# Kernel optimization log

Hardware: AMD Instinct MI355X
Metric: run time of the kernel (lower is better)

The kernel has to match this reference:

```python
import jax, jax.numpy as jnp
import numpy as np

NUM_EMBEDDINGS = 512
EMBEDDING_DIM = 64
COMMITMENT_COST = 0.25


def setup_inputs() -> dict:
    key = jax.random.key(0)
    k1, k2 = jax.random.split(key)
    inputs = jax.random.normal(k1, (64, EMBEDDING_DIM, 32, 32), dtype=jnp.float32)
    # codebook initialized uniform(-1/K, 1/K) like the torch module
    bound = 1.0 / NUM_EMBEDDINGS
    embedding = jax.random.uniform(k2, (NUM_EMBEDDINGS, EMBEDDING_DIM),
                                   dtype=jnp.float32, minval=-bound, maxval=bound)
    return {"inputs": inputs, "embedding": embedding}


def reference(inputs, embedding):
    # NCHW -> NHWC
    x = jnp.transpose(inputs, (0, 2, 3, 1))
    B, H, W, D = x.shape
    K = embedding.shape[0]
    flat = x.reshape(-1, D)  # [N, D]
    # squared L2 distances to every codebook entry: [N, K]
    dist = (jnp.sum(flat * flat, axis=1, keepdims=True)
            + jnp.sum(embedding * embedding, axis=1)
            - 2.0 * flat @ embedding.T)
    idx = jnp.argmin(dist, axis=1)  # [N]
    # gather replaces one-hot @ codebook (same math)
    quantized = embedding[idx].reshape(B, H, W, D)
    e_latent_loss = jnp.mean((jax.lax.stop_gradient(quantized) - x) ** 2)
    q_latent_loss = jnp.mean((quantized - jax.lax.stop_gradient(x)) ** 2)
    loss = q_latent_loss + COMMITMENT_COST * e_latent_loss
    # straight-through estimator
    quantized_st = x + jax.lax.stop_gradient(quantized - x)
    # perplexity from code usage histogram (== mean of one-hot encodings)
    avg_probs = jnp.zeros((K,), dtype=x.dtype).at[idx].add(1.0) / idx.shape[0]
    perplexity = jnp.exp(-jnp.sum(avg_probs * jnp.log(avg_probs + 1e-10)))
    return (loss,
            jnp.transpose(quantized_st, (0, 3, 1, 2)),
            perplexity,
            quantized_st.reshape(B, -1))
```

## Files before the change

### kernel.cpp

```cpp
#include <hip/hip_runtime.h>


constexpr int DIM    = 64;
constexpr int KC     = 512;
constexpr int HW     = 1024;
constexpr int NPTS   = 65536;
constexpr int QELEMS = NPTS * DIM;

typedef float f32x16 __attribute__((ext_vector_type(16)));
typedef short bf16x8 __attribute__((ext_vector_type(8)));

__device__ inline unsigned short f2bf(float f) {
    unsigned u = __float_as_uint(f);
    u += 0x7FFF + ((u >> 16) & 1);
    return (unsigned short)(u >> 16);
}
__device__ inline float bf2f(unsigned short s) { return __uint_as_float(((unsigned)s) << 16); }

__device__ inline uint4 pack8(const unsigned short* s) {
    return make_uint4((unsigned)s[0] | ((unsigned)s[1] << 16),
                      (unsigned)s[2] | ((unsigned)s[3] << 16),
                      (unsigned)s[4] | ((unsigned)s[5] << 16),
                      (unsigned)s[6] | ((unsigned)s[7] << 16));
}

__global__ __launch_bounds__(256)
void vq_prep_kernel(const float* __restrict__ emb, unsigned short* __restrict__ EH)
{
    const int t = blockIdx.x * 256 + threadIdx.x;
    if (t < 4096) {
        const int c = t & 511, hb = t >> 9;
        const int d0 = 16 * (hb >> 1) + 4 * (hb & 1);
        const float* e = emb + (size_t)c * DIM;
        float4 v0 = *reinterpret_cast<const float4*>(e + d0);
        float4 v1 = *reinterpret_cast<const float4*>(e + d0 + 8);
        unsigned short s[8];
        s[0]=f2bf(-v0.x); s[1]=f2bf(-v0.y); s[2]=f2bf(-v0.z); s[3]=f2bf(-v0.w);
        s[4]=f2bf(-v1.x); s[5]=f2bf(-v1.y); s[6]=f2bf(-v1.z); s[7]=f2bf(-v1.w);
        *reinterpret_cast<uint4*>(EH + (size_t)(hb * KC + c) * 8) = pack8(s);
    } else if (t < 4608) {
        const int c = t - 4096;
        const float4* er = reinterpret_cast<const float4*>(emb + (size_t)c * DIM);
        float nrm = 0.f;
        #pragma unroll
        for (int i = 0; i < DIM / 4; ++i) {
            float4 v = er[i];
            nrm = fmaf(v.x,v.x,fmaf(v.y,v.y,fmaf(v.z,v.z,fmaf(v.w,v.w,nrm))));
        }
        float val = 0.5f + 0.5f * nrm;
        unsigned short nh = f2bf(val);
        unsigned short nl = f2bf(val - bf2f(nh));
        unsigned short ext[8] = {nh, nl, 0,0,0,0,0,0};
        unsigned short zer[8] = {0,0,0,0,0,0,0,0};
        *reinterpret_cast<uint4*>(EH + (size_t)(8 * KC + c) * 8) = pack8(ext);
        *reinterpret_cast<uint4*>(EH + (size_t)(9 * KC + c) * 8) = pack8(zer);
    }
}

__global__ __launch_bounds__(256, 4)
void vq_main_kernel(const float* __restrict__ x, const float* __restrict__ emb,
                    const unsigned short* __restrict__ EH,
                    int* __restrict__ hist, float* __restrict__ loss_accum,
                    float* __restrict__ out_nchw, float* __restrict__ out_flat)
{
    __shared__ unsigned wkeys[4][32];

    const int tid  = threadIdx.x;
    const int w    = tid >> 6, lane = tid & 63;
    const int lo   = lane & 31, hi = lane >> 5;
    const int pair = w >> 1,  pw  = w & 1;

    const int n0  = blockIdx.x * 64 + pair * 32;
    const int b   = n0 >> 10;
    const int hw0 = n0 & (HW - 1);

    bf16x8 BH[4], BL[4];
    float xnorm = 0.f;
    const float* xp = x + (size_t)b * (DIM * HW) + hw0 + lo;
    #pragma unroll
    for (int ks = 0; ks < 4; ++ks) {
        bf16x8 bh, bl;
        #pragma unroll
        for (int j = 0; j < 8; ++j) {
            const int d = 16 * ks + 4 * hi + (j & 3) + 8 * (j >> 2);
            float v = xp[(size_t)d * HW];
            xnorm = fmaf(v, v, xnorm);
            unsigned short h = f2bf(v);
            bh[j] = (short)h;
            bl[j] = (short)f2bf(v - bf2f(h));
        }
        BH[ks] = bh; BL[ks] = bl;
    }
    bf16x8 B1 = {(short)0x3F80, (short)0x3F80, 0,0,0,0,0,0};

    unsigned rkey = 0xFFFFFFFFu;
    const int cbase = pw * 256;
    #pragma unroll
    for (int cc = 0; cc < 4; ++cc) {
        const int c0 = cbase + 64 * cc;
        f32x16 a0 = {}, a1 = {};
        #pragma unroll
        for (int ks = 0; ks < 4; ++ks) {
            const int hb = 2 * ks + hi;
            bf16x8 A0 = *reinterpret_cast<const bf16x8*>(EH + (size_t)(hb * KC + c0 + lo) * 8);
            bf16x8 A1 = *reinterpret_cast<const bf16x8*>(EH + (size_t)(hb * KC + c0 + 32 + lo) * 8);
            a0 = __builtin_amdgcn_mfma_f32_32x32x16_bf16(A0, BH[ks], a0, 0, 0, 0);
            a1 = __builtin_amdgcn_mfma_f32_32x32x16_bf16(A1, BH[ks], a1, 0, 0, 0);
            a0 = __builtin_amdgcn_mfma_f32_32x32x16_bf16(A0, BL[ks], a0, 0, 0, 0);
            a1 = __builtin_amdgcn_mfma_f32_32x32x16_bf16(A1, BL[ks], a1, 0, 0, 0);
        }
        {
            const int hb = 8 + hi;
            bf16x8 N0 = *reinterpret_cast<const bf16x8*>(EH + (size_t)(hb * KC + c0 + lo) * 8);
            bf16x8 N1 = *reinterpret_cast<const bf16x8*>(EH + (size_t)(hb * KC + c0 + 32 + lo) * 8);
            a0 = __builtin_amdgcn_mfma_f32_32x32x16_bf16(N0, B1, a0, 0, 0, 0);
            a1 = __builtin_amdgcn_mfma_f32_32x32x16_bf16(N1, B1, a1, 0, 0, 0);
        }
        const unsigned kb0 = (unsigned)(c0 + 4 * hi), kb1 = kb0 + 32;
        unsigned m0 = 0xFFFFFFFFu, m1 = 0xFFFFFFFFu, m2 = 0xFFFFFFFFu, m3 = 0xFFFFFFFFu;
        #pragma unroll
        for (int r = 0; r < 16; ++r) {
            const unsigned kc = (unsigned)((r & 3) + 8 * (r >> 2));
            unsigned k0 = (__float_as_uint(a0[r]) & 0xFFFFFE00u) | (kb0 + kc);
            unsigned k1 = (__float_as_uint(a1[r]) & 0xFFFFFE00u) | (kb1 + kc);
            unsigned m  = min(k0, k1);
            if ((r & 3) == 0) m0 = min(m0, m);
            else if ((r & 3) == 1) m1 = min(m1, m);
            else if ((r & 3) == 2) m2 = min(m2, m);
            else m3 = min(m3, m);
        }
        rkey = min(rkey, min(min(m0, m1), min(m2, m3)));
    }

    rkey  = min(rkey, (unsigned)__shfl_xor((int)rkey, 32, 64));
    xnorm += __shfl_xor(xnorm, 32, 64);
    if (hi == 0) wkeys[w][lo] = rkey;
    __syncthreads();
    const unsigned fkey = min(wkeys[2 * pair][lo], wkeys[2 * pair + 1][lo]);

    if (pw == 0) {
        const int   code = (int)(fkey & 511u);
        const float v    = __uint_as_float(fkey & 0xFFFFFE00u);
        float ls = (hi == 0) ? (2.f * v - 1.f + xnorm) : 0.f;
        if (hi == 0) atomicAdd(&hist[code], 1);
        #pragma unroll
        for (int off = 32; off > 0; off >>= 1) ls += __shfl_down(ls, off, 64);
        if (lane == 0) atomicAdd(loss_accum, ls);
    }

    if (pw == 0) {
        const int p = lane >> 1, q = lane & 1;
        const int code = __shfl((int)fkey, p, 64) & 511;
        const float4* er = reinterpret_cast<const float4*>(emb + (size_t)code * DIM) + q * 8;
        float* ob = out_nchw + (size_t)b * (DIM * HW) + hw0 + p;
        #pragma unroll
        for (int j = 0; j < 8; ++j) {
            float4 vv = er[j];
            const int d = q * 32 + 4 * j;
            ob[(size_t)(d + 0) * HW] = vv.x;
            ob[(size_t)(d + 1) * HW] = vv.y;
            ob[(size_t)(d + 2) * HW] = vv.z;
            ob[(size_t)(d + 3) * HW] = vv.w;
        }
    } else {
        #pragma unroll
        for (int i = 0; i < 16; ++i) {
            const int p = 2 * i + hi;
            const int code = __shfl((int)fkey, p, 64) & 511;
            float2 vv = *reinterpret_cast<const float2*>(emb + (size_t)code * DIM + 2 * lo);
            *reinterpret_cast<float2*>(out_flat + (size_t)(n0 + p) * DIM + 2 * lo) = vv;
        }
    }
}

__global__ __launch_bounds__(512, 1)
void vq_finalize_kernel(const int* __restrict__ hist, const float* __restrict__ loss_accum,
                        float* __restrict__ out_loss, float* __restrict__ out_perp)
{
    __shared__ float wsum[8];
    const int tid = threadIdx.x;
    const float p = (float)hist[tid] * (1.0f / (float)NPTS);
    float t = p * logf(p + 1e-10f);
    #pragma unroll
    for (int off = 32; off > 0; off >>= 1)
        t += __shfl_down(t, off, 64);
    if ((tid & 63) == 0) wsum[tid >> 6] = t;
    __syncthreads();
    if (tid == 0) {
        float s = 0.f;
        #pragma unroll
        for (int w = 0; w < 8; ++w) s += wsum[w];
        *out_perp = expf(-s);
        *out_loss = (*loss_accum) * 1.25f / (float)QELEMS;
    }
}

extern "C" void kernel_launch(void* const* d_in, const int* in_sizes, int n_in,
                              void* d_out, int out_size, void* d_ws, size_t ws_size,
                              hipStream_t stream)
{
    const float* x   = (const float*)d_in[0];
    const float* emb = (const float*)d_in[1];
    float* out = (float*)d_out;

    float*          loss_accum = (float*)d_ws;
    int*            hist       = (int*)((char*)d_ws + 64);
    unsigned short* EH         = (unsigned short*)((char*)d_ws + 4096);

    hipMemsetAsync(d_ws, 0, 4096, stream);

    vq_prep_kernel<<<18, 256, 0, stream>>>(emb, EH);

    vq_main_kernel<<<NPTS / 64, 256, 0, stream>>>(x, emb, EH, hist, loss_accum,
                                                  out + 1, out + 2 + QELEMS);

    vq_finalize_kernel<<<1, 512, 0, stream>>>(hist, loss_accum, out, out + 1 + QELEMS);
}
```

Baseline: 126.3 us.

## Split VQ main kernel into argmin and output-writing kernels with LDS transpose

The fused kernel is split into an argmin kernel, which stores per-point codes to a workspace index buffer, and a separate outputs kernel that gathers codebook rows, writes the flat output, and transposes through padded shared memory for the NCHW output. The argmin kernel also hoists all x loads and codebook fragment loads ahead of the MFMA chain to expose more memory-level parallelism. This is meant to make the output stores more uniform and lighten register pressure in the compute kernel. In exchange it adds a kernel launch and an extra round trip of the index array through global memory.

```diff
diff --git a/kernel.cpp b/kernel.cpp
--- a/kernel.cpp
+++ b/kernel.cpp
@@ -58,10 +58,9 @@
 }
 
 __global__ __launch_bounds__(256, 4)
-void vq_main_kernel(const float* __restrict__ x, const float* __restrict__ emb,
-                    const unsigned short* __restrict__ EH,
-                    int* __restrict__ hist, float* __restrict__ loss_accum,
-                    float* __restrict__ out_nchw, float* __restrict__ out_flat)
+void vq_argmin_kernel(const float* __restrict__ x, const unsigned short* __restrict__ EH,
+                      int* __restrict__ idx, int* __restrict__ hist,
+                      float* __restrict__ loss_accum)
 {
     __shared__ unsigned wkeys[4][32];
 
@@ -74,16 +73,22 @@
     const int b   = n0 >> 10;
     const int hw0 = n0 & (HW - 1);
 
+    const float* xp = x + (size_t)b * (DIM * HW) + hw0 + lo;
+    float xv[32];
+    #pragma unroll
+    for (int ks = 0; ks < 4; ++ks)
+        #pragma unroll
+        for (int j = 0; j < 8; ++j)
+            xv[ks * 8 + j] = xp[(size_t)(16 * ks + 4 * hi + (j & 3) + 8 * (j >> 2)) * HW];
+
     bf16x8 BH[4], BL[4];
     float xnorm = 0.f;
-    const float* xp = x + (size_t)b * (DIM * HW) + hw0 + lo;
     #pragma unroll
     for (int ks = 0; ks < 4; ++ks) {
         bf16x8 bh, bl;
         #pragma unroll
         for (int j = 0; j < 8; ++j) {
-            const int d = 16 * ks + 4 * hi + (j & 3) + 8 * (j >> 2);
-            float v = xp[(size_t)d * HW];
+            float v = xv[ks * 8 + j];
             xnorm = fmaf(v, v, xnorm);
             unsigned short h = f2bf(v);
             bh[j] = (short)h;
@@ -98,24 +103,29 @@
     #pragma unroll
     for (int cc = 0; cc < 4; ++cc) {
         const int c0 = cbase + 64 * cc;
+        bf16x8 A0[5], A1[5];
+        #pragma unroll
+        for (int ks = 0; ks < 4; ++ks) {
+            const size_t base = (size_t)((2 * ks + hi) * KC + c0 + lo) * 8;
+            A0[ks] = *reinterpret_cast<const bf16x8*>(EH + base);
+            A1[ks] = *reinterpret_cast<const bf16x8*>(EH + base + 256);
+        }
+        {
+            const size_t base = (size_t)((8 + hi) * KC + c0 + lo) * 8;
+            A0[4] = *reinterpret_cast<const bf16x8*>(EH + base);
+            A1[4] = *reinterpret_cast<const bf16x8*>(EH + base + 256);
+        }
         f32x16 a0 = {}, a1 = {};
         #pragma unroll
         for (int ks = 0; ks < 4; ++ks) {
-            const int hb = 2 * ks + hi;
-            bf16x8 A0 = *reinterpret_cast<const bf16x8*>(EH + (size_t)(hb * KC + c0 + lo) * 8);
-            bf16x8 A1 = *reinterpret_cast<const bf16x8*>(EH + (size_t)(hb * KC + c0 + 32 + lo) * 8);
-            a0 = __builtin_amdgcn_mfma_f32_32x32x16_bf16(A0, BH[ks], a0, 0, 0, 0);
-            a1 = __builtin_amdgcn_mfma_f32_32x32x16_bf16(A1, BH[ks], a1, 0, 0, 0);
-            a0 = __builtin_amdgcn_mfma_f32_32x32x16_bf16(A0, BL[ks], a0, 0, 0, 0);
-            a1 = __builtin_amdgcn_mfma_f32_32x32x16_bf16(A1, BL[ks], a1, 0, 0, 0);
-        }
-        {
-            const int hb = 8 + hi;
-            bf16x8 N0 = *reinterpret_cast<const bf16x8*>(EH + (size_t)(hb * KC + c0 + lo) * 8);
-            bf16x8 N1 = *reinterpret_cast<const bf16x8*>(EH + (size_t)(hb * KC + c0 + 32 + lo) * 8);
-            a0 = __builtin_amdgcn_mfma_f32_32x32x16_bf16(N0, B1, a0, 0, 0, 0);
-            a1 = __builtin_amdgcn_mfma_f32_32x32x16_bf16(N1, B1, a1, 0, 0, 0);
-        }
+            a0 = __builtin_amdgcn_mfma_f32_32x32x16_bf16(A0[ks], BH[ks], a0, 0, 0, 0);
+            a1 = __builtin_amdgcn_mfma_f32_32x32x16_bf16(A1[ks], BH[ks], a1, 0, 0, 0);
+            a0 = __builtin_amdgcn_mfma_f32_32x32x16_bf16(A0[ks], BL[ks], a0, 0, 0, 0);
+            a1 = __builtin_amdgcn_mfma_f32_32x32x16_bf16(A1[ks], BL[ks], a1, 0, 0, 0);
+        }
+        a0 = __builtin_amdgcn_mfma_f32_32x32x16_bf16(A0[4], B1, a0, 0, 0, 0);
+        a1 = __builtin_amdgcn_mfma_f32_32x32x16_bf16(A1[4], B1, a1, 0, 0, 0);
+
         const unsigned kb0 = (unsigned)(c0 + 4 * hi), kb1 = kb0 + 32;
         unsigned m0 = 0xFFFFFFFFu, m1 = 0xFFFFFFFFu, m2 = 0xFFFFFFFFu, m3 = 0xFFFFFFFFu;
         #pragma unroll
@@ -132,44 +142,62 @@
         rkey = min(rkey, min(min(m0, m1), min(m2, m3)));
     }
 
-    rkey  = min(rkey, (unsigned)__shfl_xor((int)rkey, 32, 64));
+    rkey   = min(rkey, (unsigned)__shfl_xor((int)rkey, 32, 64));
     xnorm += __shfl_xor(xnorm, 32, 64);
     if (hi == 0) wkeys[w][lo] = rkey;
     __syncthreads();
-    const unsigned fkey = min(wkeys[2 * pair][lo], wkeys[2 * pair + 1][lo]);
 
     if (pw == 0) {
+        const unsigned fkey = min(wkeys[2 * pair][lo], wkeys[2 * pair + 1][lo]);
         const int   code = (int)(fkey & 511u);
         const float v    = __uint_as_float(fkey & 0xFFFFFE00u);
+        if (hi == 0) {
+            idx[n0 + lo] = code;
+            atomicAdd(&hist[code], 1);
+        }
         float ls = (hi == 0) ? (2.f * v - 1.f + xnorm) : 0.f;
-        if (hi == 0) atomicAdd(&hist[code], 1);
         #pragma unroll
         for (int off = 32; off > 0; off >>= 1) ls += __shfl_down(ls, off, 64);
         if (lane == 0) atomicAdd(loss_accum, ls);
     }
-
-    if (pw == 0) {
-        const int p = lane >> 1, q = lane & 1;
-        const int code = __shfl((int)fkey, p, 64) & 511;
-        const float4* er = reinterpret_cast<const float4*>(emb + (size_t)code * DIM) + q * 8;
+}
+
+__global__ __launch_bounds__(256)
+void vq_outputs_kernel(const float* __restrict__ emb, const int* __restrict__ idx,
+                       float* __restrict__ out_nchw, float* __restrict__ out_flat)
+{
+    __shared__ float rows[64 * 65];
+    __shared__ int   scode[64];
+
+    const int tid = threadIdx.x;
+    const int p0  = blockIdx.x * 64;
+    const int b   = p0 >> 10;
+    const int hw0 = p0 & (HW - 1);
+
+    if (tid < 64) scode[tid] = idx[p0 + tid];
+    __syncthreads();
+
+    {
+        const int p = tid >> 2, q = tid & 3;
+        const float4* er = reinterpret_cast<const float4*>(emb + (size_t)scode[p] * DIM) + q * 4;
+        float2* of = reinterpret_cast<float2*>(out_flat + (size_t)(p0 + p) * DIM + q * 16);
+        float*  dst = &rows[p * 65 + q * 16];
+        #pragma unroll
+        for (int i = 0; i < 4; ++i) {
+            float4 v = er[i];
+            of[2 * i]     = make_float2(v.x, v.y);
+            of[2 * i + 1] = make_float2(v.z, v.w);
+            dst[4 * i + 0] = v.x; dst[4 * i + 1] = v.y;
+            dst[4 * i + 2] = v.z; dst[4 * i + 3] = v.w;
+        }
+    }
+    __syncthreads();
+    {
+        const int p = tid & 63, d0 = (tid >> 6) * 16;
         float* ob = out_nchw + (size_t)b * (DIM * HW) + hw0 + p;
         #pragma unroll
-        for (int j = 0; j < 8; ++j) {
-            float4 vv = er[j];
-            const int d = q * 32 + 4 * j;
-            ob[(size_t)(d + 0) * HW] = vv.x;
-            ob[(size_t)(d + 1) * HW] = vv.y;
-            ob[(size_t)(d + 2) * HW] = vv.z;
-            ob[(size_t)(d + 3) * HW] = vv.w;
-        }
-    } else {
-        #pragma unroll
-        for (int i = 0; i < 16; ++i) {
-            const int p = 2 * i + hi;
-            const int code = __shfl((int)fkey, p, 64) & 511;
-            float2 vv = *reinterpret_cast<const float2*>(emb + (size_t)code * DIM + 2 * lo);
-            *reinterpret_cast<float2*>(out_flat + (size_t)(n0 + p) * DIM + 2 * lo) = vv;
-        }
+        for (int i = 0; i < 16; ++i)
+            ob[(size_t)(d0 + i) * HW] = rows[p * 65 + d0 + i];
     }
 }
 
@@ -206,13 +234,15 @@
     float*          loss_accum = (float*)d_ws;
     int*            hist       = (int*)((char*)d_ws + 64);
     unsigned short* EH         = (unsigned short*)((char*)d_ws + 4096);
+    int*            idx        = (int*)((char*)d_ws + 4096 + 81920);
 
     hipMemsetAsync(d_ws, 0, 4096, stream);
 
     vq_prep_kernel<<<18, 256, 0, stream>>>(emb, EH);
 
-    vq_main_kernel<<<NPTS / 64, 256, 0, stream>>>(x, emb, EH, hist, loss_accum,
-                                                  out + 1, out + 2 + QELEMS);
+    vq_argmin_kernel<<<NPTS / 64, 256, 0, stream>>>(x, EH, idx, hist, loss_accum);
+
+    vq_outputs_kernel<<<NPTS / 64, 256, 0, stream>>>(emb, idx, out + 1, out + 2 + QELEMS);
 
     vq_finalize_kernel<<<1, 512, 0, stream>>>(hist, loss_accum, out, out + 1 + QELEMS);
 }
```

Measured after the change: 133.4 us. 5.7% more time.
